# Performance work log

Measured on AMD Instinct MI355X. Metric: run time of the kernel, lower is better.

The kernel has to match this reference:

```python
import jax, jax.numpy as jnp
import numpy as np
import math

B, S, DIM, HEADS, HEAD_DIM = 2, 2048, 1024, 16, 64
ROT_DIM, ROPE_THETA = 64, 10000.0


def make_rope(seq_len):
    # DitRotary.forward: theta over half rotary_dim, duplicated interleaved pairs
    theta = 1.0 / (ROPE_THETA ** (np.arange(0, ROT_DIM, 2, dtype=np.float32) / ROT_DIM))
    pos = np.arange(seq_len, dtype=np.float32).reshape(-1, 1)
    idx = pos * theta  # [S, 32]
    cos = np.stack((np.cos(idx), np.cos(idx)), axis=-1).reshape(seq_len, -1)  # [S, 64]
    sin = np.stack((np.sin(idx), np.sin(idx)), axis=-1).reshape(seq_len, -1)
    # unsqueeze(2).unsqueeze(1) -> [1, S, 1, 64]
    return jnp.asarray(cos)[None, :, None, :], jnp.asarray(sin)[None, :, None, :]


def rotate_half(x):
    # interleaved-pair rotation: (x1, x2) -> (-x2, x1)
    x = x.reshape(*x.shape[:-1], -1, 2)
    x1, x2 = x[..., 0], x[..., 1]
    return jnp.stack((-x2, x1), axis=-1).reshape(*x.shape[:-2], -1)


def apply_rotary(x, cos, sin):
    return x * cos + rotate_half(x) * sin


def setup_inputs() -> dict:
    key = jax.random.key(0)
    ks = jax.random.split(key, 8)
    sc = 1.0 / math.sqrt(DIM)
    x = jax.random.normal(ks[0], (B, S, DIM), dtype=jnp.float32)
    cos, sin = make_rope(S)
    Wq = jax.random.normal(ks[1], (DIM, DIM), dtype=jnp.float32) * sc
    bq = jnp.zeros((DIM,), jnp.float32)
    Wk = jax.random.normal(ks[2], (DIM, DIM), dtype=jnp.float32) * sc
    bk = jnp.zeros((DIM,), jnp.float32)
    Wv = jax.random.normal(ks[3], (DIM, DIM), dtype=jnp.float32) * sc
    bv = jnp.zeros((DIM,), jnp.float32)
    Wo = jax.random.normal(ks[4], (DIM, DIM), dtype=jnp.float32) * sc
    bo = jnp.zeros((DIM,), jnp.float32)
    mask = jnp.ones((B, 1, 1, S), dtype=bool)
    return {"x": x, "cos": cos, "sin": sin, "Wq": Wq, "bq": bq, "Wk": Wk,
            "bk": bk, "Wv": Wv, "bv": bv, "Wo": Wo, "bo": bo, "mask": mask}


def reference(x, cos, sin, Wq, bq, Wk, bk, Wv, bv, Wo, bo, mask):
    b, s, _ = x.shape
    q = (x @ Wq.T + bq).reshape(b, s, HEADS, HEAD_DIM)
    k = (x @ Wk.T + bk).reshape(b, s, HEADS, HEAD_DIM)
    v = (x @ Wv.T + bv).reshape(b, s, HEADS, HEAD_DIM)
    # partial rotary: applied only to head index 0 (dim 2 of [B,S,H,D])
    q = jnp.concatenate([apply_rotary(q[:, :, :1, :], cos, sin), q[:, :, 1:, :]], axis=2)
    k = jnp.concatenate([apply_rotary(k[:, :, :1, :], cos, sin), k[:, :, 1:, :]], axis=2)
    # [B,H,S,D]
    q = q.transpose(0, 2, 1, 3)
    k = k.transpose(0, 2, 1, 3)
    v = v.transpose(0, 2, 1, 3)
    neg = jnp.finfo(jnp.float32).min
    attn_mask = jnp.where(mask, 0.0, neg)  # ~mask * finfo.min
    scores = jnp.einsum("bhsd,bhtd->bhst", q, k) / math.sqrt(HEAD_DIM)
    scores = scores + attn_mask
    probs = jax.nn.softmax(scores.astype(jnp.float32), axis=-1).astype(q.dtype)
    out = jnp.einsum("bhst,bhtd->bhsd", probs, v)
    out = out.transpose(0, 2, 1, 3).reshape(b, s, HEADS * HEAD_DIM)
    return out @ Wo.T + bo
```

## Files before the change

kernel.cpp:

```cpp
#include <hip/hip_runtime.h>
#include <hip/hip_bf16.h>


typedef __attribute__((ext_vector_type(8))) __bf16 bf16x8;
typedef __attribute__((ext_vector_type(4))) __bf16 bf16x4;
typedef __attribute__((ext_vector_type(4))) float f32x4;
typedef __attribute__((ext_vector_type(4))) short s16x4;

#define NB_B 2
#define NB_S 2048
#define NB_DIM 1024
#define NB_H 16
#define NB_HD 64
#define NB_BS (NB_B * NB_S)

__device__ __forceinline__ void async_cp16(const __bf16* g, __bf16* l) {
    __builtin_amdgcn_global_load_lds(
        (const __attribute__((address_space(1))) unsigned int*)g,
        (__attribute__((address_space(3))) unsigned int*)l, 16, 0, 0);
}

__global__ __launch_bounds__(256) void cvt_kernel(
    const float* __restrict__ x,  const float* __restrict__ wq,
    const float* __restrict__ wk, const float* __restrict__ wv,
    __bf16* __restrict__ xb,  __bf16* __restrict__ wqb,
    __bf16* __restrict__ wkb, __bf16* __restrict__ wvb) {
    const int XQ = (NB_BS * NB_DIM) / 4;
    const int WQ = (NB_DIM * NB_DIM) / 4;
    int i = blockIdx.x * 256 + threadIdx.x;
    const float* src; __bf16* dst; int off;
    if (i < XQ)              { src = x;  dst = xb;  off = i; }
    else if (i < XQ + WQ)    { src = wq; dst = wqb; off = i - XQ; }
    else if (i < XQ + 2*WQ)  { src = wk; dst = wkb; off = i - XQ - WQ; }
    else                     { src = wv; dst = wvb; off = i - XQ - 2*WQ; }
    f32x4 v = *(const f32x4*)(src + (size_t)off * 4);
    bf16x4 b;
#pragma unroll
    for (int j = 0; j < 4; ++j) b[j] = (__bf16)v[j];
    *(bf16x4*)(dst + (size_t)off * 4) = b;
}

__global__ __launch_bounds__(256) void gemm_qkv_kernel(
    const __bf16* __restrict__ A,
    const float* __restrict__ cosb, const float* __restrict__ sinb,
    const __bf16* __restrict__ Wq, const float* __restrict__ bq, __bf16* __restrict__ qbuf,
    const __bf16* __restrict__ Wk, const float* __restrict__ bk, __bf16* __restrict__ kbuf,
    const __bf16* __restrict__ Wv, const float* __restrict__ bv, __bf16* __restrict__ vtbuf) {
    constexpr int K = 1024;
    __shared__ __align__(16) __bf16 As[128][64];
    __shared__ __align__(16) __bf16 Bs[128][64];

    const int z = blockIdx.z;
    const __bf16* W; const float* bias;
    if (z == 0)      { W = Wq; bias = bq; }
    else if (z == 1) { W = Wk; bias = bk; }
    else             { W = Wv; bias = bv; }

    const int tid = threadIdx.x;
    const int lane = tid & 63;
    const int w = tid >> 6;
    const int wm = w >> 1, wn = w & 1;
    const int row16 = lane & 15, quad = lane >> 4;
    const int r7 = row16 & 7;
    const int m0 = blockIdx.x * 128, n0 = blockIdx.y * 128;

    f32x4 acc[4][4] = {};

    for (int kt = 0; kt < K; kt += 64) {
        __syncthreads();
#pragma unroll
        for (int i = 0; i < 4; ++i) {
            int c = tid + i * 256;
            int row = c >> 3, g = c & 7;
            int gcol = (g ^ (row & 7)) << 3;
            async_cp16(A + (size_t)(m0 + row) * K + kt + gcol, &As[row][g << 3]);
            async_cp16(W + (size_t)(n0 + row) * K + kt + gcol, &Bs[row][g << 3]);
        }
        __syncthreads();

        bf16x8 af[4][2], bfr[4][2];
#pragma unroll
        for (int t = 0; t < 4; ++t)
#pragma unroll
            for (int kk = 0; kk < 2; ++kk) {
                af[t][kk]  = *(const bf16x8*)&As[wm * 64 + t * 16 + row16][((kk * 4 + quad) ^ r7) << 3];
                bfr[t][kk] = *(const bf16x8*)&Bs[wn * 64 + t * 16 + row16][((kk * 4 + quad) ^ r7) << 3];
            }
        __builtin_amdgcn_s_setprio(1);
#pragma unroll
        for (int mt = 0; mt < 4; ++mt)
#pragma unroll
            for (int nt = 0; nt < 4; ++nt)
#pragma unroll
                for (int kk = 0; kk < 2; ++kk)
                    acc[mt][nt] = __builtin_amdgcn_mfma_f32_16x16x32_bf16(af[mt][kk], bfr[nt][kk], acc[mt][nt], 0, 0, 0);
        __builtin_amdgcn_s_setprio(0);
    }

    if (z == 2) {
#pragma unroll
        for (int mt = 0; mt < 4; ++mt) {
            int row = m0 + wm * 64 + mt * 16 + quad * 4;
            int b = row >> 11, s = row & (NB_S - 1);
#pragma unroll
            for (int nt = 0; nt < 4; ++nt) {
                int col = n0 + wn * 64 + nt * 16 + row16;
                float bv = bias[col];
                bf16x4 pack;
#pragma unroll
                for (int r = 0; r < 4; ++r) pack[r] = (__bf16)(acc[mt][nt][r] + bv);
                *(bf16x4*)&vtbuf[(size_t)b * (NB_DIM * NB_S) + (size_t)col * NB_S + s] = pack;
            }
        }
    } else {
        __bf16* C = (z == 0) ? qbuf : kbuf;
        const bool rope = (n0 == 0) && (wn == 0);
#pragma unroll
        for (int mt = 0; mt < 4; ++mt) {
            int row = m0 + wm * 64 + mt * 16 + quad * 4;
#pragma unroll
            for (int nt = 0; nt < 4; ++nt) {
                int col = n0 + wn * 64 + nt * 16 + row16;
                float bv = bias[col];
#pragma unroll
                for (int r = 0; r < 4; ++r) {
                    float val = acc[mt][nt][r] + bv;
                    if (rope) {
                        float part = __shfl_xor(val, 1, 64);
                        int srow = (row + r) & (NB_S - 1);
                        float c  = cosb[srow * 64 + col];
                        float sn = sinb[srow * 64 + col];
                        val = (lane & 1) ? (val * c + part * sn) : (val * c - part * sn);
                    }
                    C[(size_t)(row + r) * NB_DIM + col] = (__bf16)val;
                }
            }
        }
    }
}

__global__ __launch_bounds__(256) void gemm_o_kernel(
    const __bf16* __restrict__ A, const float* __restrict__ W,
    const float* __restrict__ bias, float* __restrict__ C) {
    constexpr int K = 1024;
    __shared__ __align__(16) __bf16 As[128][64];
    __shared__ __align__(16) __bf16 Bs[64][64];

    const int tid = threadIdx.x;
    const int lane = tid & 63;
    const int w = tid >> 6;
    const int row16 = lane & 15, quad = lane >> 4;
    const int r7 = row16 & 7;
    const int m0 = blockIdx.x * 128, n0 = blockIdx.y * 64;

    f32x4 acc[2][4] = {};
    f32x4 breg[4];

    auto load_b = [&](int kt) {
#pragma unroll
        for (int i = 0; i < 4; ++i) {
            int s = tid + i * 256;
            int row = s >> 4, f4 = s & 15;
            breg[i] = *(const f32x4*)(W + (size_t)(n0 + row) * K + kt + f4 * 4);
        }
    };

    load_b(0);
    for (int kt = 0; kt < K; kt += 64) {
        __syncthreads();
#pragma unroll
        for (int i = 0; i < 4; ++i) {
            int c = tid + i * 256;
            int row = c >> 3, g = c & 7;
            int gcol = (g ^ (row & 7)) << 3;
            async_cp16(A + (size_t)(m0 + row) * K + kt + gcol, &As[row][g << 3]);
        }
#pragma unroll
        for (int i = 0; i < 4; ++i) {
            int s = tid + i * 256;
            int row = s >> 4, f4 = s & 15;
            int g = f4 >> 1, sub = f4 & 1;
            int co = ((g ^ (row & 7)) << 3) + sub * 4;
            bf16x4 bv;
#pragma unroll
            for (int j = 0; j < 4; ++j) bv[j] = (__bf16)breg[i][j];
            *(bf16x4*)&Bs[row][co] = bv;
        }
        __syncthreads();
        if (kt + 64 < K) load_b(kt + 64);

        bf16x8 af[2][2], bfr[4][2];
#pragma unroll
        for (int t = 0; t < 2; ++t)
#pragma unroll
            for (int kk = 0; kk < 2; ++kk)
                af[t][kk] = *(const bf16x8*)&As[w * 32 + t * 16 + row16][((kk * 4 + quad) ^ r7) << 3];
#pragma unroll
        for (int nt = 0; nt < 4; ++nt)
#pragma unroll
            for (int kk = 0; kk < 2; ++kk)
                bfr[nt][kk] = *(const bf16x8*)&Bs[nt * 16 + row16][((kk * 4 + quad) ^ r7) << 3];
        __builtin_amdgcn_s_setprio(1);
#pragma unroll
        for (int mt = 0; mt < 2; ++mt)
#pragma unroll
            for (int nt = 0; nt < 4; ++nt)
#pragma unroll
                for (int kk = 0; kk < 2; ++kk)
                    acc[mt][nt] = __builtin_amdgcn_mfma_f32_16x16x32_bf16(af[mt][kk], bfr[nt][kk], acc[mt][nt], 0, 0, 0);
        __builtin_amdgcn_s_setprio(0);
    }

#pragma unroll
    for (int mt = 0; mt < 2; ++mt) {
        int row = m0 + w * 32 + mt * 16 + quad * 4;
#pragma unroll
        for (int nt = 0; nt < 4; ++nt) {
            int col = n0 + nt * 16 + row16;
            float bv = bias[col];
#pragma unroll
            for (int r = 0; r < 4; ++r)
                C[(size_t)(row + r) * NB_DIM + col] = acc[mt][nt][r] + bv;
        }
    }
}

__global__ __launch_bounds__(512) void attn_kernel(const __bf16* __restrict__ qb,
                                                   const __bf16* __restrict__ kb,
                                                   const __bf16* __restrict__ vtb,
                                                   __bf16* __restrict__ ob) {
    __shared__ __align__(16) __bf16 Ks[2][128][72];
    __shared__ __align__(16) __bf16 Vts[2][64][132];

    const int tid = threadIdx.x;
    const int lane = tid & 63;
    const int w = tid >> 6;
    const int row16 = lane & 15, quad = lane >> 4;
    const int bh = blockIdx.x;
    const int b = bh >> 4, h = bh & 15;
    const int q0 = blockIdx.y * 256 + w * 32;

    const size_t headoff = (size_t)b * NB_S * NB_DIM + (size_t)h * NB_HD;
    const size_t vtoff = (size_t)b * (NB_DIM * NB_S) + (size_t)(h * NB_HD) * NB_S;

    const float qscale = 0.18033688011112042f;
    bf16x8 qf[2][2];
#pragma unroll
    for (int m = 0; m < 2; ++m)
#pragma unroll
        for (int hh = 0; hh < 2; ++hh) {
            bf16x8 v = *(const bf16x8*)(qb + headoff + (size_t)(q0 + m * 16 + row16) * NB_DIM + hh * 32 + quad * 8);
#pragma unroll
            for (int j = 0; j < 8; ++j) v[j] = (__bf16)((float)v[j] * qscale);
            qf[m][hh] = v;
        }

    f32x4 o[2][4] = {};
    f32x4 ol[2] = {};

    const __bf16 oneb = __builtin_bit_cast(__bf16, (short)0x3F80);
    bf16x8 ones8;
#pragma unroll
    for (int j = 0; j < 8; ++j) ones8[j] = oneb;

    bf16x8 kreg[2], vreg[2];
#pragma unroll
    for (int i = 0; i < 2; ++i) {
        int c = tid + i * 512;
        kreg[i] = *(const bf16x8*)(kb + headoff + (size_t)(c >> 3) * NB_DIM + ((c & 7) << 3));
        vreg[i] = *(const bf16x8*)(vtb + vtoff + (size_t)(c >> 4) * NB_S + ((c & 15) << 3));
    }
#pragma unroll
    for (int i = 0; i < 2; ++i) {
        int c = tid + i * 512;
        *(bf16x8*)&Ks[0][c >> 3][(c & 7) << 3] = kreg[i];
        bf16x4 lo, hi;
#pragma unroll
        for (int j = 0; j < 4; ++j) { lo[j] = vreg[i][j]; hi[j] = vreg[i][j + 4]; }
        *(bf16x4*)&Vts[0][c >> 4][(c & 15) << 3] = lo;
        *(bf16x4*)&Vts[0][c >> 4][((c & 15) << 3) + 4] = hi;
    }
#pragma unroll
    for (int i = 0; i < 2; ++i) {
        int c = tid + i * 512;
        kreg[i] = *(const bf16x8*)(kb + headoff + (size_t)(128 + (c >> 3)) * NB_DIM + ((c & 7) << 3));
        vreg[i] = *(const bf16x8*)(vtb + vtoff + (size_t)(c >> 4) * NB_S + 128 + ((c & 15) << 3));
    }
    asm volatile("s_waitcnt lgkmcnt(0)" ::: "memory");
    __builtin_amdgcn_s_barrier();

    for (int kt = 0; kt < 16; ++kt) {
        const int cur = kt & 1;
        if (kt < 15) {
#pragma unroll
            for (int i = 0; i < 2; ++i) {
                int c = tid + i * 512;
                *(bf16x8*)&Ks[cur ^ 1][c >> 3][(c & 7) << 3] = kreg[i];
                bf16x4 lo, hi;
#pragma unroll
                for (int j = 0; j < 4; ++j) { lo[j] = vreg[i][j]; hi[j] = vreg[i][j + 4]; }
                *(bf16x4*)&Vts[cur ^ 1][c >> 4][(c & 15) << 3] = lo;
                *(bf16x4*)&Vts[cur ^ 1][c >> 4][((c & 15) << 3) + 4] = hi;
            }
        }
        if (kt < 14) {
            int base = (kt + 2) * 128;
#pragma unroll
            for (int i = 0; i < 2; ++i) {
                int c = tid + i * 512;
                kreg[i] = *(const bf16x8*)(kb + headoff + (size_t)(base + (c >> 3)) * NB_DIM + ((c & 7) << 3));
                vreg[i] = *(const bf16x8*)(vtb + vtoff + (size_t)(c >> 4) * NB_S + base + ((c & 15) << 3));
            }
        }

        bf16x8 pf8[2][4];
#pragma unroll
        for (int t = 0; t < 8; ++t) {
            f32x4 s0 = {}, s1 = {};
            __builtin_amdgcn_s_setprio(1);
#pragma unroll
            for (int hh = 0; hh < 2; ++hh) {
                bf16x8 kf = *(const bf16x8*)&Ks[cur][t * 16 + row16][hh * 32 + quad * 8];
                s0 = __builtin_amdgcn_mfma_f32_16x16x32_bf16(kf, qf[0][hh], s0, 0, 0, 0);
                s1 = __builtin_amdgcn_mfma_f32_16x16x32_bf16(kf, qf[1][hh], s1, 0, 0, 0);
            }
            __builtin_amdgcn_s_setprio(0);
#pragma unroll
            for (int r = 0; r < 4; ++r) {
                pf8[0][t >> 1][(t & 1) * 4 + r] = (__bf16)__builtin_amdgcn_exp2f(s0[r]);
                pf8[1][t >> 1][(t & 1) * 4 + r] = (__bf16)__builtin_amdgcn_exp2f(s1[r]);
            }
        }

        __builtin_amdgcn_s_setprio(1);
#pragma unroll
        for (int tp = 0; tp < 4; ++tp) {
            ol[0] = __builtin_amdgcn_mfma_f32_16x16x32_bf16(pf8[0][tp], ones8, ol[0], 0, 0, 0);
            ol[1] = __builtin_amdgcn_mfma_f32_16x16x32_bf16(pf8[1][tp], ones8, ol[1], 0, 0, 0);
        }
#pragma unroll
        for (int nt = 0; nt < 4; ++nt)
#pragma unroll
            for (int tp = 0; tp < 4; ++tp) {
                bf16x4 vlo = *(const bf16x4*)&Vts[cur][nt * 16 + row16][tp * 32 + quad * 4];
                bf16x4 vhi = *(const bf16x4*)&Vts[cur][nt * 16 + row16][tp * 32 + 16 + quad * 4];
                bf16x8 vfp;
#pragma unroll
                for (int j = 0; j < 4; ++j) { vfp[j] = vlo[j]; vfp[4 + j] = vhi[j]; }
                o[0][nt] = __builtin_amdgcn_mfma_f32_16x16x32_bf16(pf8[0][tp], vfp, o[0][nt], 0, 0, 0);
                o[1][nt] = __builtin_amdgcn_mfma_f32_16x16x32_bf16(pf8[1][tp], vfp, o[1][nt], 0, 0, 0);
            }
        __builtin_amdgcn_s_setprio(0);

        if (kt < 15) {
            asm volatile("s_waitcnt lgkmcnt(0)" ::: "memory");
            __builtin_amdgcn_s_barrier();
        }
    }

#pragma unroll
    for (int m = 0; m < 2; ++m)
#pragma unroll
        for (int r = 0; r < 4; ++r) {
            float inv = 1.f / ol[m][r];
            int row = q0 + m * 16 + quad * 4 + r;
#pragma unroll
            for (int nt = 0; nt < 4; ++nt)
                ob[headoff + (size_t)row * NB_DIM + nt * 16 + row16] = (__bf16)(o[m][nt][r] * inv);
        }
}

extern "C" void kernel_launch(void* const* d_in, const int* in_sizes, int n_in,
                              void* d_out, int out_size, void* d_ws, size_t ws_size,
                              hipStream_t stream) {
    const float* x    = (const float*)d_in[0];
    const float* cosb = (const float*)d_in[1];
    const float* sinb = (const float*)d_in[2];
    const float* Wq   = (const float*)d_in[3];
    const float* bq   = (const float*)d_in[4];
    const float* Wk   = (const float*)d_in[5];
    const float* bk   = (const float*)d_in[6];
    const float* Wv   = (const float*)d_in[7];
    const float* bv   = (const float*)d_in[8];
    const float* Wo   = (const float*)d_in[9];
    const float* bo   = (const float*)d_in[10];

    __bf16* qbuf  = (__bf16*)d_ws;
    __bf16* kbuf  = qbuf + (size_t)NB_BS * NB_DIM;
    __bf16* vtbuf = kbuf + (size_t)NB_BS * NB_DIM;
    __bf16* abuf  = vtbuf + (size_t)NB_BS * NB_DIM;
    __bf16* xb    = abuf + (size_t)NB_BS * NB_DIM;
    __bf16* wqb   = xb + (size_t)NB_BS * NB_DIM;
    __bf16* wkb   = wqb + (size_t)NB_DIM * NB_DIM;
    __bf16* wvb   = wkb + (size_t)NB_DIM * NB_DIM;

    const int XQ = (NB_BS * NB_DIM) / 4, WQ = (NB_DIM * NB_DIM) / 4;
    cvt_kernel<<<(XQ + 3 * WQ) / 256, 256, 0, stream>>>(x, Wq, Wk, Wv,
                                                        xb, wqb, wkb, wvb);

    dim3 gqkv(NB_BS / 128, NB_DIM / 128, 3);
    gemm_qkv_kernel<<<gqkv, 256, 0, stream>>>(xb, cosb, sinb,
                                              wqb, bq, qbuf,
                                              wkb, bk, kbuf,
                                              wvb, bv, vtbuf);

    attn_kernel<<<dim3(NB_B * NB_H, NB_S / 256), 512, 0, stream>>>(qbuf, kbuf, vtbuf, abuf);

    dim3 go(NB_BS / 128, NB_DIM / 64);
    gemm_o_kernel<<<go, 256, 0, stream>>>(abuf, Wo, bo, (float*)d_out);
}
```

Baseline: 192.4 us.

## Fuse conversion, QKV GEMM, attention and output GEMM into one cooperative kernel

Replaces the four separate launches with a single persistent cooperative kernel of 512 blocks that runs bf16 conversion, QKV projection with RoPE, attention, and the output projection as phases separated by grid-wide syncs. This is meant to remove per-launch overhead and inter-kernel gaps. The trade-offs are grid barrier costs, a fixed grid that splits QKV tiles unevenly (some blocks do two tiles), and the occupancy limits of a shared LDS allocation. A fallback to the original multi-kernel path is kept in case the cooperative launch fails.

```diff
diff --git a/kernel.cpp b/kernel.cpp
--- a/kernel.cpp
+++ b/kernel.cpp
@@ -1,11 +1,13 @@
 #include <hip/hip_runtime.h>
 #include <hip/hip_bf16.h>
-
+#include <hip/hip_cooperative_groups.h>
+
+
+namespace cg = cooperative_groups;
 
 typedef __attribute__((ext_vector_type(8))) __bf16 bf16x8;
 typedef __attribute__((ext_vector_type(4))) __bf16 bf16x4;
 typedef __attribute__((ext_vector_type(4))) float f32x4;
-typedef __attribute__((ext_vector_type(4))) short s16x4;
 
 #define NB_B 2
 #define NB_S 2048
@@ -18,6 +20,361 @@
     __builtin_amdgcn_global_load_lds(
         (const __attribute__((address_space(1))) unsigned int*)g,
         (__attribute__((address_space(3))) unsigned int*)l, 16, 0, 0);
+}
+
+__global__ __launch_bounds__(256, 2) void fused_kernel(
+    const float* __restrict__ x,
+    const float* __restrict__ cosb, const float* __restrict__ sinb,
+    const float* __restrict__ Wq, const float* __restrict__ bq,
+    const float* __restrict__ Wk, const float* __restrict__ bk,
+    const float* __restrict__ Wv, const float* __restrict__ bv,
+    const float* __restrict__ Wo, const float* __restrict__ bo,
+    float* __restrict__ out,
+    __bf16* __restrict__ qbuf, __bf16* __restrict__ kbuf,
+    __bf16* __restrict__ vtbuf, __bf16* __restrict__ abuf,
+    __bf16* __restrict__ xb, __bf16* __restrict__ wqb,
+    __bf16* __restrict__ wkb, __bf16* __restrict__ wvb) {
+    cg::grid_group grid = cg::this_grid();
+    __shared__ __align__(16) unsigned char smem[70656];
+
+    const int tid = threadIdx.x;
+    const int lane = tid & 63;
+    const int w = tid >> 6;
+    const int row16 = lane & 15, quad = lane >> 4;
+    const int r7 = row16 & 7;
+    const int bx = blockIdx.x;
+
+    {
+        const int XQ = (NB_BS * NB_DIM) / 4;
+        const int WQ = (NB_DIM * NB_DIM) / 4;
+        const int TOT = XQ + 3 * WQ;
+        for (int base = 0; base < TOT; base += 512 * 256) {
+            int i = base + bx * 256 + tid;
+            const float* src; __bf16* dst; int off;
+            if (i < XQ)              { src = x;  dst = xb;  off = i; }
+            else if (i < XQ + WQ)    { src = Wq; dst = wqb; off = i - XQ; }
+            else if (i < XQ + 2*WQ)  { src = Wk; dst = wkb; off = i - XQ - WQ; }
+            else                     { src = Wv; dst = wvb; off = i - XQ - 2*WQ; }
+            f32x4 v = *(const f32x4*)(src + (size_t)off * 4);
+            bf16x4 b;
+#pragma unroll
+            for (int j = 0; j < 4; ++j) b[j] = (__bf16)v[j];
+            *(bf16x4*)(dst + (size_t)off * 4) = b;
+        }
+    }
+    __threadfence();
+    grid.sync();
+
+    {
+        auto As = (__bf16(*)[64])(smem);
+        auto Bs = (__bf16(*)[64])(smem + 16384);
+        constexpr int K = 1024;
+        const int wm = w >> 1, wn = w & 1;
+        const int nrep = (bx < 256) ? 2 : 1;
+        for (int rep = 0; rep < nrep; ++rep) {
+            const int t = (rep == 0) ? bx : 512 + bx;
+            const int z = t >> 8;
+            const int xy = t & 255;
+            const int m0 = (xy >> 3) * 128, n0 = (xy & 7) * 128;
+            const __bf16* W; const float* bias;
+            if (z == 0)      { W = wqb; bias = bq; }
+            else if (z == 1) { W = wkb; bias = bk; }
+            else             { W = wvb; bias = bv; }
+
+            f32x4 acc[4][4] = {};
+            for (int kt = 0; kt < K; kt += 64) {
+                __syncthreads();
+#pragma unroll
+                for (int i = 0; i < 4; ++i) {
+                    int c = tid + i * 256;
+                    int row = c >> 3, g = c & 7;
+                    int gcol = (g ^ (row & 7)) << 3;
+                    async_cp16(xb + (size_t)(m0 + row) * K + kt + gcol, &As[row][g << 3]);
+                    async_cp16(W + (size_t)(n0 + row) * K + kt + gcol, &Bs[row][g << 3]);
+                }
+                __syncthreads();
+
+                bf16x8 af[4][2], bfr[4][2];
+#pragma unroll
+                for (int tt = 0; tt < 4; ++tt)
+#pragma unroll
+                    for (int kk = 0; kk < 2; ++kk) {
+                        af[tt][kk]  = *(const bf16x8*)&As[wm * 64 + tt * 16 + row16][((kk * 4 + quad) ^ r7) << 3];
+                        bfr[tt][kk] = *(const bf16x8*)&Bs[wn * 64 + tt * 16 + row16][((kk * 4 + quad) ^ r7) << 3];
+                    }
+                __builtin_amdgcn_s_setprio(1);
+#pragma unroll
+                for (int mt = 0; mt < 4; ++mt)
+#pragma unroll
+                    for (int nt = 0; nt < 4; ++nt)
+#pragma unroll
+                        for (int kk = 0; kk < 2; ++kk)
+                            acc[mt][nt] = __builtin_amdgcn_mfma_f32_16x16x32_bf16(af[mt][kk], bfr[nt][kk], acc[mt][nt], 0, 0, 0);
+                __builtin_amdgcn_s_setprio(0);
+            }
+
+            if (z == 2) {
+#pragma unroll
+                for (int mt = 0; mt < 4; ++mt) {
+                    int row = m0 + wm * 64 + mt * 16 + quad * 4;
+                    int b = row >> 11, s = row & (NB_S - 1);
+#pragma unroll
+                    for (int nt = 0; nt < 4; ++nt) {
+                        int col = n0 + wn * 64 + nt * 16 + row16;
+                        float bvv = bias[col];
+                        bf16x4 pack;
+#pragma unroll
+                        for (int r = 0; r < 4; ++r) pack[r] = (__bf16)(acc[mt][nt][r] + bvv);
+                        *(bf16x4*)&vtbuf[(size_t)b * (NB_DIM * NB_S) + (size_t)col * NB_S + s] = pack;
+                    }
+                }
+            } else {
+                __bf16* C = (z == 0) ? qbuf : kbuf;
+                const bool rope = (n0 == 0) && (wn == 0);
+#pragma unroll
+                for (int mt = 0; mt < 4; ++mt) {
+                    int row = m0 + wm * 64 + mt * 16 + quad * 4;
+#pragma unroll
+                    for (int nt = 0; nt < 4; ++nt) {
+                        int col = n0 + wn * 64 + nt * 16 + row16;
+                        float bvv = bias[col];
+#pragma unroll
+                        for (int r = 0; r < 4; ++r) {
+                            float val = acc[mt][nt][r] + bvv;
+                            if (rope) {
+                                float part = __shfl_xor(val, 1, 64);
+                                int srow = (row + r) & (NB_S - 1);
+                                float c  = cosb[srow * 64 + col];
+                                float sn = sinb[srow * 64 + col];
+                                val = (lane & 1) ? (val * c + part * sn) : (val * c - part * sn);
+                            }
+                            C[(size_t)(row + r) * NB_DIM + col] = (__bf16)val;
+                        }
+                    }
+                }
+            }
+            __syncthreads();
+        }
+    }
+    __threadfence();
+    grid.sync();
+
+    {
+        auto Ks  = (__bf16(*)[128][72])(smem);
+        auto Vts = (__bf16(*)[64][132])(smem + 36864);
+        const int bh = bx & 31;
+        const int b = bh >> 4, h = bh & 15;
+        const int q0 = (bx >> 5) * 128 + w * 32;
+
+        const size_t headoff = (size_t)b * NB_S * NB_DIM + (size_t)h * NB_HD;
+        const size_t vtoff = (size_t)b * (NB_DIM * NB_S) + (size_t)(h * NB_HD) * NB_S;
+
+        const float qscale = 0.18033688011112042f;
+        bf16x8 qf[2][2];
+#pragma unroll
+        for (int m = 0; m < 2; ++m)
+#pragma unroll
+            for (int hh = 0; hh < 2; ++hh) {
+                bf16x8 v = *(const bf16x8*)(qbuf + headoff + (size_t)(q0 + m * 16 + row16) * NB_DIM + hh * 32 + quad * 8);
+#pragma unroll
+                for (int j = 0; j < 8; ++j) v[j] = (__bf16)((float)v[j] * qscale);
+                qf[m][hh] = v;
+            }
+
+        f32x4 o[2][4] = {};
+        f32x4 ol[2] = {};
+
+        const __bf16 oneb = __builtin_bit_cast(__bf16, (short)0x3F80);
+        bf16x8 ones8;
+#pragma unroll
+        for (int j = 0; j < 8; ++j) ones8[j] = oneb;
+
+        bf16x8 kreg[4], vreg[4];
+#pragma unroll
+        for (int i = 0; i < 4; ++i) {
+            int c = tid + i * 256;
+            kreg[i] = *(const bf16x8*)(kbuf + headoff + (size_t)(c >> 3) * NB_DIM + ((c & 7) << 3));
+            vreg[i] = *(const bf16x8*)(vtbuf + vtoff + (size_t)(c >> 4) * NB_S + ((c & 15) << 3));
+        }
+#pragma unroll
+        for (int i = 0; i < 4; ++i) {
+            int c = tid + i * 256;
+            *(bf16x8*)&Ks[0][c >> 3][(c & 7) << 3] = kreg[i];
+            bf16x4 lo, hi;
+#pragma unroll
+            for (int j = 0; j < 4; ++j) { lo[j] = vreg[i][j]; hi[j] = vreg[i][j + 4]; }
+            *(bf16x4*)&Vts[0][c >> 4][(c & 15) << 3] = lo;
+            *(bf16x4*)&Vts[0][c >> 4][((c & 15) << 3) + 4] = hi;
+        }
+#pragma unroll
+        for (int i = 0; i < 4; ++i) {
+            int c = tid + i * 256;
+            kreg[i] = *(const bf16x8*)(kbuf + headoff + (size_t)(128 + (c >> 3)) * NB_DIM + ((c & 7) << 3));
+            vreg[i] = *(const bf16x8*)(vtbuf + vtoff + (size_t)(c >> 4) * NB_S + 128 + ((c & 15) << 3));
+        }
+        asm volatile("s_waitcnt lgkmcnt(0)" ::: "memory");
+        __builtin_amdgcn_s_barrier();
+
+        for (int kt = 0; kt < 16; ++kt) {
+            const int cur = kt & 1;
+            if (kt < 15) {
+#pragma unroll
+                for (int i = 0; i < 4; ++i) {
+                    int c = tid + i * 256;
+                    *(bf16x8*)&Ks[cur ^ 1][c >> 3][(c & 7) << 3] = kreg[i];
+                    bf16x4 lo, hi;
+#pragma unroll
+                    for (int j = 0; j < 4; ++j) { lo[j] = vreg[i][j]; hi[j] = vreg[i][j + 4]; }
+                    *(bf16x4*)&Vts[cur ^ 1][c >> 4][(c & 15) << 3] = lo;
+                    *(bf16x4*)&Vts[cur ^ 1][c >> 4][((c & 15) << 3) + 4] = hi;
+                }
+            }
+            if (kt < 14) {
+                int base = (kt + 2) * 128;
+#pragma unroll
+                for (int i = 0; i < 4; ++i) {
+                    int c = tid + i * 256;
+                    kreg[i] = *(const bf16x8*)(kbuf + headoff + (size_t)(base + (c >> 3)) * NB_DIM + ((c & 7) << 3));
+                    vreg[i] = *(const bf16x8*)(vtbuf + vtoff + (size_t)(c >> 4) * NB_S + base + ((c & 15) << 3));
+                }
+            }
+
+            bf16x8 pf8[2][4];
+#pragma unroll
+            for (int t = 0; t < 8; ++t) {
+                f32x4 s0 = {}, s1 = {};
+                __builtin_amdgcn_s_setprio(1);
+#pragma unroll
+                for (int hh = 0; hh < 2; ++hh) {
+                    bf16x8 kf = *(const bf16x8*)&Ks[cur][t * 16 + row16][hh * 32 + quad * 8];
+                    s0 = __builtin_amdgcn_mfma_f32_16x16x32_bf16(kf, qf[0][hh], s0, 0, 0, 0);
+                    s1 = __builtin_amdgcn_mfma_f32_16x16x32_bf16(kf, qf[1][hh], s1, 0, 0, 0);
+                }
+                __builtin_amdgcn_s_setprio(0);
+#pragma unroll
+                for (int r = 0; r < 4; ++r) {
+                    pf8[0][t >> 1][(t & 1) * 4 + r] = (__bf16)__builtin_amdgcn_exp2f(s0[r]);
+                    pf8[1][t >> 1][(t & 1) * 4 + r] = (__bf16)__builtin_amdgcn_exp2f(s1[r]);
+                }
+            }
+
+            __builtin_amdgcn_s_setprio(1);
+#pragma unroll
+            for (int tp = 0; tp < 4; ++tp) {
+                ol[0] = __builtin_amdgcn_mfma_f32_16x16x32_bf16(pf8[0][tp], ones8, ol[0], 0, 0, 0);
+                ol[1] = __builtin_amdgcn_mfma_f32_16x16x32_bf16(pf8[1][tp], ones8, ol[1], 0, 0, 0);
+            }
+#pragma unroll
+            for (int nt = 0; nt < 4; ++nt)
+#pragma unroll
+                for (int tp = 0; tp < 4; ++tp) {
+                    bf16x4 vlo = *(const bf16x4*)&Vts[cur][nt * 16 + row16][tp * 32 + quad * 4];
+                    bf16x4 vhi = *(const bf16x4*)&Vts[cur][nt * 16 + row16][tp * 32 + 16 + quad * 4];
+                    bf16x8 vfp;
+#pragma unroll
+                    for (int j = 0; j < 4; ++j) { vfp[j] = vlo[j]; vfp[4 + j] = vhi[j]; }
+                    o[0][nt] = __builtin_amdgcn_mfma_f32_16x16x32_bf16(pf8[0][tp], vfp, o[0][nt], 0, 0, 0);
+                    o[1][nt] = __builtin_amdgcn_mfma_f32_16x16x32_bf16(pf8[1][tp], vfp, o[1][nt], 0, 0, 0);
+                }
+            __builtin_amdgcn_s_setprio(0);
+
+            if (kt < 15) {
+                asm volatile("s_waitcnt lgkmcnt(0)" ::: "memory");
+                __builtin_amdgcn_s_barrier();
+            }
+        }
+
+#pragma unroll
+        for (int m = 0; m < 2; ++m)
+#pragma unroll
+            for (int r = 0; r < 4; ++r) {
+                float inv = 1.f / ol[m][r];
+                int row = q0 + m * 16 + quad * 4 + r;
+#pragma unroll
+                for (int nt = 0; nt < 4; ++nt)
+                    abuf[headoff + (size_t)row * NB_DIM + nt * 16 + row16] = (__bf16)(o[m][nt][r] * inv);
+            }
+    }
+    __threadfence();
+    grid.sync();
+
+    {
+        auto As = (__bf16(*)[64])(smem);
+        auto Bs = (__bf16(*)[64])(smem + 16384);
+        constexpr int K = 1024;
+        const int m0 = (bx >> 4) * 128, n0 = (bx & 15) * 64;
+
+        f32x4 acc[2][4] = {};
+        f32x4 breg[4];
+
+        auto load_b = [&](int kt) {
+#pragma unroll
+            for (int i = 0; i < 4; ++i) {
+                int s = tid + i * 256;
+                int row = s >> 4, f4 = s & 15;
+                breg[i] = *(const f32x4*)(Wo + (size_t)(n0 + row) * K + kt + f4 * 4);
+            }
+        };
+
+        load_b(0);
+        for (int kt = 0; kt < K; kt += 64) {
+            __syncthreads();
+#pragma unroll
+            for (int i = 0; i < 4; ++i) {
+                int c = tid + i * 256;
+                int row = c >> 3, g = c & 7;
+                int gcol = (g ^ (row & 7)) << 3;
+                async_cp16(abuf + (size_t)(m0 + row) * K + kt + gcol, &As[row][g << 3]);
+            }
+#pragma unroll
+            for (int i = 0; i < 4; ++i) {
+                int s = tid + i * 256;
+                int row = s >> 4, f4 = s & 15;
+                int g = f4 >> 1, sub = f4 & 1;
+                int co = ((g ^ (row & 7)) << 3) + sub * 4;
+                bf16x4 bv;
+#pragma unroll
+                for (int j = 0; j < 4; ++j) bv[j] = (__bf16)breg[i][j];
+                *(bf16x4*)&Bs[row][co] = bv;
+            }
+            __syncthreads();
+            if (kt + 64 < K) load_b(kt + 64);
+
+            bf16x8 af[2][2], bfr[4][2];
+#pragma unroll
+            for (int t = 0; t < 2; ++t)
+#pragma unroll
+                for (int kk = 0; kk < 2; ++kk)
+                    af[t][kk] = *(const bf16x8*)&As[w * 32 + t * 16 + row16][((kk * 4 + quad) ^ r7) << 3];
+#pragma unroll
+            for (int nt = 0; nt < 4; ++nt)
+#pragma unroll
+                for (int kk = 0; kk < 2; ++kk)
+                    bfr[nt][kk] = *(const bf16x8*)&Bs[nt * 16 + row16][((kk * 4 + quad) ^ r7) << 3];
+            __builtin_amdgcn_s_setprio(1);
+#pragma unroll
+            for (int mt = 0; mt < 2; ++mt)
+#pragma unroll
+                for (int nt = 0; nt < 4; ++nt)
+#pragma unroll
+                    for (int kk = 0; kk < 2; ++kk)
+                        acc[mt][nt] = __builtin_amdgcn_mfma_f32_16x16x32_bf16(af[mt][kk], bfr[nt][kk], acc[mt][nt], 0, 0, 0);
+            __builtin_amdgcn_s_setprio(0);
+        }
+
+#pragma unroll
+        for (int mt = 0; mt < 2; ++mt) {
+            int row = m0 + w * 32 + mt * 16 + quad * 4;
+#pragma unroll
+            for (int nt = 0; nt < 4; ++nt) {
+                int col = n0 + nt * 16 + row16;
+                float bvv = bo[col];
+#pragma unroll
+                for (int r = 0; r < 4; ++r)
+                    out[(size_t)(row + r) * NB_DIM + col] = acc[mt][nt][r] + bvv;
+            }
+        }
+    }
 }
 
 __global__ __launch_bounds__(256) void cvt_kernel(
@@ -384,6 +741,7 @@
     const float* bv   = (const float*)d_in[8];
     const float* Wo   = (const float*)d_in[9];
     const float* bo   = (const float*)d_in[10];
+    float* out        = (float*)d_out;
 
     __bf16* qbuf  = (__bf16*)d_ws;
     __bf16* kbuf  = qbuf + (size_t)NB_BS * NB_DIM;
@@ -394,18 +752,29 @@
     __bf16* wkb   = wqb + (size_t)NB_DIM * NB_DIM;
     __bf16* wvb   = wkb + (size_t)NB_DIM * NB_DIM;
 
-    const int XQ = (NB_BS * NB_DIM) / 4, WQ = (NB_DIM * NB_DIM) / 4;
-    cvt_kernel<<<(XQ + 3 * WQ) / 256, 256, 0, stream>>>(x, Wq, Wk, Wv,
-                                                        xb, wqb, wkb, wvb);
-
-    dim3 gqkv(NB_BS / 128, NB_DIM / 128, 3);
-    gemm_qkv_kernel<<<gqkv, 256, 0, stream>>>(xb, cosb, sinb,
-                                              wqb, bq, qbuf,
-                                              wkb, bk, kbuf,
-                                              wvb, bv, vtbuf);
-
-    attn_kernel<<<dim3(NB_B * NB_H, NB_S / 256), 512, 0, stream>>>(qbuf, kbuf, vtbuf, abuf);
-
-    dim3 go(NB_BS / 128, NB_DIM / 64);
-    gemm_o_kernel<<<go, 256, 0, stream>>>(abuf, Wo, bo, (float*)d_out);
+    void* args[] = {
+        (void*)&x, (void*)&cosb, (void*)&sinb,
+        (void*)&Wq, (void*)&bq, (void*)&Wk, (void*)&bk,
+        (void*)&Wv, (void*)&bv, (void*)&Wo, (void*)&bo,
+        (void*)&out,
+        (void*)&qbuf, (void*)&kbuf, (void*)&vtbuf, (void*)&abuf,
+        (void*)&xb, (void*)&wqb, (void*)&wkb, (void*)&wvb
+    };
+    hipError_t err = hipLaunchCooperativeKernel(
+        (const void*)fused_kernel, dim3(512), dim3(256), args, 0, stream);
+
+    if (err != hipSuccess) {
+        (void)hipGetLastError();
+        const int XQ = (NB_BS * NB_DIM) / 4, WQ = (NB_DIM * NB_DIM) / 4;
+        cvt_kernel<<<(XQ + 3 * WQ) / 256, 256, 0, stream>>>(x, Wq, Wk, Wv,
+                                                            xb, wqb, wkb, wvb);
+        dim3 gqkv(NB_BS / 128, NB_DIM / 128, 3);
+        gemm_qkv_kernel<<<gqkv, 256, 0, stream>>>(xb, cosb, sinb,
+                                                  wqb, bq, qbuf,
+                                                  wkb, bk, kbuf,
+                                                  wvb, bv, vtbuf);
+        attn_kernel<<<dim3(NB_B * NB_H, NB_S / 256), 512, 0, stream>>>(qbuf, kbuf, vtbuf, abuf);
+        dim3 go(NB_BS / 128, NB_DIM / 64);
+        gemm_o_kernel<<<go, 256, 0, stream>>>(abuf, Wo, bo, out);
+    }
 }
```

Result: slower. 554.5 us (+188.3%).
